# Kernel optimization log

Hardware: AMD Instinct MI355X
Metric: run time of the kernel (lower is better)

The kernel has to match this reference:

```python
import jax, jax.numpy as jnp
import numpy as np

N = 50000      # nodes
E = 1_600_000  # edges (avg degree 32)
IN, H, OUT, R = 128, 64, 32, 8
NEG_SLOPE = 0.2


def _rgat(x, src, dst, etype, W, q, k, b, n_nodes):
    """PyG RGATConv, defaults: heads=1, dim=1, additive-self-attention,
    across-relation softmax, concat=True, bias=True, dropout=0 (eval)."""
    # per-relation transform of all nodes: [R, N, O] (cheaper than per-edge bmm since 2*deg >> R)
    t = jnp.einsum('ni,rio->rno', x, W)
    xi = t[etype, dst]                      # [E, O] transformed target feats
    xj = t[etype, src]                      # [E, O] transformed source feats
    a = (xi @ q + xj @ k)[:, 0]             # [E] additive attention logits
    a = jnp.where(a >= 0, a, NEG_SLOPE * a)  # leaky_relu
    # segment softmax over incoming edges of each target node (across relations)
    m = jax.ops.segment_max(a, dst, num_segments=n_nodes)
    m = jnp.where(jnp.isfinite(m), m, 0.0)
    ex = jnp.exp(a - m[dst])
    s = jax.ops.segment_sum(ex, dst, num_segments=n_nodes)
    alpha = ex / (s[dst] + 1e-16)
    out = jax.ops.segment_sum(alpha[:, None] * xj, dst, num_segments=n_nodes)
    return out + b


def setup_inputs() -> dict:
    key = jax.random.key(0)
    ks = jax.random.split(key, 24)
    x = jax.random.normal(ks[0], (N, IN), jnp.float32)
    edge_index = jax.random.randint(ks[1], (2, E), 0, N, jnp.int32)
    edge_type = jax.random.randint(ks[2], (E,), 0, R, jnp.int32)

    def glorot(k, shape, fan_in):
        return jax.random.normal(k, shape, jnp.float32) * (1.0 / np.sqrt(fan_in))

    d = dict(x=x, edge_index=edge_index, edge_type=edge_type)
    # conv1: in->hidden, conv_mu / conv_logvar: hidden->hidden
    d['W1'] = glorot(ks[3], (R, IN, H), IN)
    d['q1'] = glorot(ks[4], (H, 1), H)
    d['k1'] = glorot(ks[5], (H, 1), H)
    d['b1'] = jnp.zeros((H,), jnp.float32)
    d['Wmu'] = glorot(ks[6], (R, H, H), H)
    d['qmu'] = glorot(ks[7], (H, 1), H)
    d['kmu'] = glorot(ks[8], (H, 1), H)
    d['bmu'] = jnp.zeros((H,), jnp.float32)
    d['Wlv'] = glorot(ks[9], (R, H, H), H)
    d['qlv'] = glorot(ks[10], (H, 1), H)
    d['klv'] = glorot(ks[11], (H, 1), H)
    d['blv'] = jnp.zeros((H,), jnp.float32)
    d['Wm'] = glorot(ks[12], (H, OUT), H)   # linear_mu (stored [in,out])
    d['bm'] = jnp.zeros((OUT,), jnp.float32)
    d['Wl'] = glorot(ks[13], (H, OUT), H)   # linear_logvar
    d['bl'] = jnp.zeros((OUT,), jnp.float32)
    return d


def reference(x, edge_index, edge_type, W1, q1, k1, b1,
              Wmu, qmu, kmu, bmu, Wlv, qlv, klv, blv, Wm, bm, Wl, bl):
    src, dst = edge_index[0], edge_index[1]
    hidden = jax.nn.relu(_rgat(x, src, dst, edge_type, W1, q1, k1, b1, N))
    mu = jax.nn.relu(_rgat(hidden, src, dst, edge_type, Wmu, qmu, kmu, bmu, N))
    mu = mu @ Wm + bm                       # dropout is identity in eval
    logvar = jax.nn.relu(_rgat(hidden, src, dst, edge_type, Wlv, qlv, klv, blv, N))
    logvar = logvar @ Wl + bl
    logstd = 0.5 * logvar
    return (mu, logstd)
```

## Files before the change

### kernel.cpp

```cpp
#include <hip/hip_runtime.h>
#include <cstdint>

#define HDIM 64
#define ODIM 32
#define NEG_SLOPE 0.2f
#define SCHUNK 2048
#define EPB 8192

typedef __attribute__((ext_vector_type(8))) short v8s;
typedef __attribute__((ext_vector_type(4))) float v4f;

__device__ __forceinline__ unsigned f2bf_rne(float f) {
  unsigned u = __float_as_uint(f);
  return (u + 0x7FFFu + ((u >> 16) & 1u)) >> 16;
}

__device__ __forceinline__ unsigned fenc(float f) {
  unsigned u = __float_as_uint(f);
  return (u & 0x80000000u) ? ~u : (u | 0x80000000u);
}
__device__ __forceinline__ float fdec(unsigned e) {
  unsigned u = (e & 0x80000000u) ? (e ^ 0x80000000u) : ~e;
  return __uint_as_float(u);
}

__global__ __launch_bounds__(256) void cvt_bf16_kernel(
    const float* __restrict__ in, unsigned short* __restrict__ out, int n) {
  int i = (blockIdx.x * 256 + threadIdx.x) * 4;
  if (i + 3 < n) {
    float4 v = *(const float4*)&in[i];
    ushort4 o;
    o.x = (unsigned short)f2bf_rne(v.x);
    o.y = (unsigned short)f2bf_rne(v.y);
    o.z = (unsigned short)f2bf_rne(v.z);
    o.w = (unsigned short)f2bf_rne(v.w);
    *(ushort4*)&out[i] = o;
  }
}

__global__ __launch_bounds__(256) void transpose_w_kernel(
    const float* __restrict__ W1, const float* __restrict__ Wmu,
    const float* __restrict__ Wlv, unsigned short* __restrict__ W1t,
    unsigned short* __restrict__ Wmut, unsigned short* __restrict__ Wlvt) {
  const int b = blockIdx.x;
  const int r = b & 7;
  const int which = b >> 3;
  const float* src;
  unsigned short* dst;
  int K;
  if (which == 0) {
    src = W1; dst = W1t; K = 128;
  } else if (which == 1) {
    src = Wmu; dst = Wmut; K = 64;
  } else {
    src = Wlv; dst = Wlvt; K = 64;
  }
  for (int idx = threadIdx.x; idx < K * 64; idx += 256) {
    const int kk = idx >> 6, o = idx & 63;
    dst[((size_t)r * 64 + o) * K + kk] =
        (unsigned short)f2bf_rne(src[((size_t)r * K + kk) * 64 + o]);
  }
}

__global__ __launch_bounds__(256) void count_deg_kernel(
    const int* __restrict__ dst, int* __restrict__ deg, int E) {
  int e = blockIdx.x * 256 + threadIdx.x;
  if (e < E) atomicAdd(&deg[dst[e]], 1);
}

__global__ __launch_bounds__(256) void scan_p1(const int* __restrict__ deg,
                                               int* __restrict__ bsum, int n) {
  int base = blockIdx.x * SCHUNK + threadIdx.x * 8;
  int s = 0;
#pragma unroll
  for (int j = 0; j < 8; j++) {
    int i = base + j;
    if (i < n) s += deg[i];
  }
#pragma unroll
  for (int d = 1; d < 64; d <<= 1) s += __shfl_xor(s, d, 64);
  __shared__ int ws[4];
  if ((threadIdx.x & 63) == 0) ws[threadIdx.x >> 6] = s;
  __syncthreads();
  if (threadIdx.x == 0) bsum[blockIdx.x] = ws[0] + ws[1] + ws[2] + ws[3];
}

__global__ void scan_p2(int* bsum, int nb) {
  int i = threadIdx.x;
  int v = (i < nb) ? bsum[i] : 0;
  int orig = v;
#pragma unroll
  for (int d = 1; d < 64; d <<= 1) {
    int up = __shfl_up(v, d, 64);
    if (i >= d) v += up;
  }
  if (i < nb) bsum[i] = v - orig;
}

__global__ __launch_bounds__(256) void scan_p3(const int* __restrict__ deg,
                                               const int* __restrict__ bsum,
                                               int* __restrict__ row_ptr,
                                               int n) {
  int base = blockIdx.x * SCHUNK + threadIdx.x * 8;
  int vals[8];
  int s = 0;
#pragma unroll
  for (int j = 0; j < 8; j++) {
    int i = base + j;
    vals[j] = (i < n) ? deg[i] : 0;
    s += vals[j];
  }
  int lane = threadIdx.x & 63, w = threadIdx.x >> 6;
  int v = s;
#pragma unroll
  for (int d = 1; d < 64; d <<= 1) {
    int up = __shfl_up(v, d, 64);
    if (lane >= d) v += up;
  }
  __shared__ int wsum[4];
  if (lane == 63) wsum[w] = v;
  __syncthreads();
  int woff = 0;
#pragma unroll
  for (int i = 0; i < 4; i++) woff += (i < w) ? wsum[i] : 0;
  int off = bsum[blockIdx.x] + woff + v - s;
#pragma unroll
  for (int j = 0; j < 8; j++) {
    int i = base + j;
    off += vals[j];
    if (i < n) row_ptr[i + 1] = off;
  }
  if (blockIdx.x == 0 && threadIdx.x == 0) row_ptr[0] = 0;
}

__global__ __launch_bounds__(256) void bucket_cursor_init(
    const int* __restrict__ row_ptr, int* __restrict__ cursor, int N, int nb) {
  int i = threadIdx.x;
  if (i < nb) cursor[i] = row_ptr[min(i * 256, N)];
}

__global__ __launch_bounds__(256) void bucket_pass1(
    const int* __restrict__ src, const int* __restrict__ dst,
    const int* __restrict__ etype, int* __restrict__ cursor,
    unsigned* __restrict__ tmp, int E) {
  __shared__ int hist[256];
  __shared__ int binstart[256];
  __shared__ int gbase[256];
  __shared__ int fill[256];
  __shared__ int wsum[4];
  __shared__ unsigned stage[EPB];
  __shared__ unsigned char binof[EPB];
  const int tid = threadIdx.x;
  const int e0 = blockIdx.x * EPB;
  const int cnt = min(EPB, E - e0);

  hist[tid] = 0;
  fill[tid] = 0;
  __syncthreads();
  for (int j = tid; j < cnt; j += 256) atomicAdd(&hist[dst[e0 + j] >> 8], 1);
  __syncthreads();

  const int hv = hist[tid];
  {
    const int lane = tid & 63, w = tid >> 6;
    int iv = hv;
#pragma unroll
    for (int d = 1; d < 64; d <<= 1) {
      int up = __shfl_up(iv, d, 64);
      if (lane >= d) iv += up;
    }
    if (lane == 63) wsum[w] = iv;
    __syncthreads();
    int woff = 0;
#pragma unroll
    for (int i = 0; i < 4; i++) woff += (i < w) ? wsum[i] : 0;
    binstart[tid] = woff + iv - hv;
    if (hv > 0) gbase[tid] = atomicAdd(&cursor[tid], hv);
  }
  __syncthreads();

  for (int j = tid; j < cnt; j += 256) {
    const int d = dst[e0 + j];
    const int b = d >> 8;
    const unsigned rec = ((unsigned)(d & 255) << 19) |
                         ((unsigned)etype[e0 + j] << 16) |
                         (unsigned)src[e0 + j];
    const int slot = binstart[b] + atomicAdd(&fill[b], 1);
    stage[slot] = rec;
    binof[slot] = (unsigned char)b;
  }
  __syncthreads();

  for (int s = tid; s < cnt; s += 256) {
    const int b = binof[s];
    tmp[gbase[b] + (s - binstart[b])] = stage[s];
  }
}

__global__ __launch_bounds__(256) void bucket_pass2(
    const int* __restrict__ row_ptr, const unsigned* __restrict__ tmp,
    int* __restrict__ edges, int N) {
  __shared__ int rp[257];
  __shared__ int fill[256];
  const int tid = threadIdx.x;
  const int rowbase = blockIdx.x * 256;
  const int rowcnt = min(256, N - rowbase);
  for (int i = tid; i <= rowcnt; i += 256) rp[i] = row_ptr[rowbase + i];
  fill[tid] = 0;
  __syncthreads();
  const int beg = rp[0];
  const int endv = rp[rowcnt];
  for (int i = beg + tid; i < endv; i += 256) {
    const unsigned rec = tmp[i];
    const int dlow = rec >> 19;
    const int pos = rp[dlow] + atomicAdd(&fill[dlow], 1);
    edges[pos] = (int)(rec & 0x7FFFFu);
  }
}

__global__ __launch_bounds__(256) void rowmax_kernel(
    const float* __restrict__ ak, unsigned* __restrict__ maxk_enc, int N) {
  const int row = blockIdx.x;
  const int nchunks = gridDim.y;
  const int per = (N + nchunks - 1) / nchunks;
  const int beg = blockIdx.y * per;
  const int end = min(N, beg + per);
  const float* r = ak + (size_t)row * N;
  float m = -1e30f;
  for (int i = beg + threadIdx.x; i < end; i += 256) m = fmaxf(m, r[i]);
#pragma unroll
  for (int d = 1; d < 64; d <<= 1) m = fmaxf(m, __shfl_xor(m, d, 64));
  __shared__ float ws[4];
  if ((threadIdx.x & 63) == 0) ws[threadIdx.x >> 6] = m;
  __syncthreads();
  if (threadIdx.x == 0) {
    float bm = fmaxf(fmaxf(ws[0], ws[1]), fmaxf(ws[2], ws[3]));
    atomicMax(&maxk_enc[row], fenc(bm));
  }
}

__global__ __launch_bounds__(256) void transform1_mfma(
    const unsigned short* __restrict__ xb,
    const unsigned short* __restrict__ W1t, const float* __restrict__ q,
    const float* __restrict__ k, unsigned short* __restrict__ tb,
    float* __restrict__ aq, float* __restrict__ ak, int N) {
  __shared__ unsigned short st[4][16][72];
  const int r = blockIdx.x;
  const int tid = threadIdx.x;
  const int w = tid >> 6;
  const int lane = tid & 63;
  const int quad = lane >> 4;
  const int mrow = lane & 15;
  const int n0w = blockIdx.y * 64 + w * 16;

  const int gA = min(n0w + mrow, N - 1);
  const unsigned short* arow = xb + (size_t)gA * 128 + quad * 8;
  const unsigned short* wrow = W1t + ((size_t)r * 64 + mrow) * 128 + quad * 8;

  v4f acc[4];
#pragma unroll
  for (int tt = 0; tt < 4; tt++) acc[tt] = (v4f){0.f, 0.f, 0.f, 0.f};

#pragma unroll
  for (int k0 = 0; k0 < 128; k0 += 32) {
    v8s a = *(const v8s*)(arow + k0);
#pragma unroll
    for (int tt = 0; tt < 4; tt++) {
      v8s b = *(const v8s*)(wrow + (size_t)tt * 16 * 128 + k0);
      acc[tt] = __builtin_amdgcn_mfma_f32_16x16x32_bf16(a, b, acc[tt], 0, 0, 0);
    }
  }

  float qv[4], kv[4];
#pragma unroll
  for (int tt = 0; tt < 4; tt++) {
    qv[tt] = q[tt * 16 + mrow];
    kv[tt] = k[tt * 16 + mrow];
  }

#pragma unroll
  for (int i = 0; i < 4; i++) {
    float vq = 0.f, vk = 0.f;
#pragma unroll
    for (int tt = 0; tt < 4; tt++) {
      vq = fmaf(acc[tt][i], qv[tt], vq);
      vk = fmaf(acc[tt][i], kv[tt], vk);
      st[w][quad * 4 + i][tt * 16 + mrow] =
          (unsigned short)f2bf_rne(acc[tt][i]);
    }
#pragma unroll
    for (int d = 1; d < 16; d <<= 1) {
      vq += __shfl_xor(vq, d, 64);
      vk += __shfl_xor(vk, d, 64);
    }
    const int gn = n0w + quad * 4 + i;
    if (mrow == 0 && gn < N) {
      aq[(size_t)r * N + gn] = vq;
      ak[(size_t)r * N + gn] = vk;
    }
  }
  __syncthreads();

  const int row = lane >> 2, cg = lane & 3;
  const int gns = n0w + row;
  if (gns < N) {
    const uint4 v0 = *(const uint4*)&st[w][row][cg * 16];
    const uint4 v1 = *(const uint4*)&st[w][row][cg * 16 + 8];
    uint4* dst = (uint4*)&tb[((size_t)r * N + gns) * 64 + cg * 16];
    dst[0] = v0;
    dst[1] = v1;
  }
}

__global__ __launch_bounds__(256) void transform2_mfma(
    const unsigned short* __restrict__ hb,
    const unsigned short* __restrict__ Wmut,
    const unsigned short* __restrict__ Wlvt, const float* __restrict__ qa,
    const float* __restrict__ ka, const float* __restrict__ qb,
    const float* __restrict__ kb, unsigned* __restrict__ t2p,
    float* __restrict__ aq2, float* __restrict__ ak2, int N) {
  __shared__ unsigned st2[4][16][68];
  const int r = blockIdx.x;
  const int tid = threadIdx.x;
  const int w = tid >> 6;
  const int lane = tid & 63;
  const int quad = lane >> 4;
  const int mrow = lane & 15;
  const int n0w = blockIdx.y * 64 + w * 16;

  const int gA = min(n0w + mrow, N - 1);
  const unsigned short* arow = hb + (size_t)gA * 64 + quad * 8;
  const size_t woff = ((size_t)r * 64 + mrow) * 64 + quad * 8;

  v4f am[4], al[4];
#pragma unroll
  for (int tt = 0; tt < 4; tt++) {
    am[tt] = (v4f){0.f, 0.f, 0.f, 0.f};
    al[tt] = (v4f){0.f, 0.f, 0.f, 0.f};
  }

#pragma unroll
  for (int k0 = 0; k0 < 64; k0 += 32) {
    v8s a = *(const v8s*)(arow + k0);
#pragma unroll
    for (int tt = 0; tt < 4; tt++) {
      v8s bm = *(const v8s*)(Wmut + woff + (size_t)tt * 16 * 64 + k0);
      v8s bl = *(const v8s*)(Wlvt + woff + (size_t)tt * 16 * 64 + k0);
      am[tt] = __builtin_amdgcn_mfma_f32_16x16x32_bf16(a, bm, am[tt], 0, 0, 0);
      al[tt] = __builtin_amdgcn_mfma_f32_16x16x32_bf16(a, bl, al[tt], 0, 0, 0);
    }
  }

  float qmv[4], kmv[4], qlv2[4], klv2[4];
#pragma unroll
  for (int tt = 0; tt < 4; tt++) {
    qmv[tt] = qa[tt * 16 + mrow];
    kmv[tt] = ka[tt * 16 + mrow];
    qlv2[tt] = qb[tt * 16 + mrow];
    klv2[tt] = kb[tt * 16 + mrow];
  }

#pragma unroll
  for (int i = 0; i < 4; i++) {
    float vqm = 0.f, vkm = 0.f, vql = 0.f, vkl = 0.f;
#pragma unroll
    for (int tt = 0; tt < 4; tt++) {
      vqm = fmaf(am[tt][i], qmv[tt], vqm);
      vkm = fmaf(am[tt][i], kmv[tt], vkm);
      vql = fmaf(al[tt][i], qlv2[tt], vql);
      vkl = fmaf(al[tt][i], klv2[tt], vkl);
      st2[w][quad * 4 + i][tt * 16 + mrow] =
          f2bf_rne(am[tt][i]) | (f2bf_rne(al[tt][i]) << 16);
    }
#pragma unroll
    for (int d = 1; d < 16; d <<= 1) {
      vqm += __shfl_xor(vqm, d, 64);
      vkm += __shfl_xor(vkm, d, 64);
      vql += __shfl_xor(vql, d, 64);
      vkl += __shfl_xor(vkl, d, 64);
    }
    const int gn = n0w + quad * 4 + i;
    if (mrow == 0 && gn < N) {
      aq2[(size_t)r * N + gn] = vqm;
      ak2[(size_t)r * N + gn] = vkm;
      aq2[(size_t)(8 + r) * N + gn] = vql;
      ak2[(size_t)(8 + r) * N + gn] = vkl;
    }
  }
  __syncthreads();

  const int row = lane >> 2, cg = lane & 3;
  const int gns = n0w + row;
  if (gns < N) {
    unsigned* dst = &t2p[((size_t)r * N + gns) * 64 + cg * 16];
#pragma unroll
    for (int s = 0; s < 4; s++)
      *(uint4*)(dst + s * 4) = *(const uint4*)&st2[w][row][cg * 16 + s * 4];
  }
}

__global__ __launch_bounds__(256) void aggregate_kernel(
    const int* __restrict__ row_ptr, const int* __restrict__ edges,
    const unsigned short* __restrict__ tb, const float* __restrict__ aq,
    const float* __restrict__ ak, const unsigned* __restrict__ maxk_enc,
    const float* __restrict__ bias, unsigned short* __restrict__ hb, int N) {
  const int tid = threadIdx.x;
  const int w = tid >> 6, o = tid & 63;
  int wid = blockIdx.x * 4 + w;
  const bool valid = wid < N;
  if (!valid) wid = N - 1;
  const int beg = row_ptr[wid];
  const int end = valid ? row_ptr[wid + 1] : beg;
  const int deg = end - beg;

  const float aqw = aq[(size_t)(o & 7) * N + wid];

  float v = aqw + fdec(maxk_enc[o & 7]);
  v = (v >= 0.f) ? v : NEG_SLOPE * v;
#pragma unroll
  for (int d = 1; d < 8; d <<= 1) v = fmaxf(v, __shfl_xor(v, d, 64));
  const float m = __shfl(v, 0, 64);

  const int g = o >> 3;
  const int cl = o & 7;
  float s = 0.f;
  float acc[8];
#pragma unroll
  for (int c = 0; c < 8; c++) acc[c] = 0.f;

  for (int base = 0; base < deg; base += 64) {
    const int j = base + o;
    const int gcount = min(64, deg - base);
    const int packed = edges[beg + min(j, deg - 1)];
    const int src = packed & 0xFFFF;
    const int rr = packed >> 16;
    const int idx = rr * N + src;
    float x = __shfl(aqw, rr, 64) + ak[idx];
    x = (x >= 0.f) ? x : NEG_SLOPE * x;
    const float p = (j < deg) ? __expf(x - m) : 0.f;
    s += p;
    const int g8 = (gcount + 7) & ~7;
#pragma unroll 4
    for (int u = 0; u < g8; u += 8) {
      const int e = u + g;
      const float pe = __shfl(p, e, 64);
      const int ie = __shfl(idx, e, 64);
      const uint4 tv = *(const uint4*)(tb + (size_t)ie * 64 + cl * 8);
      const unsigned uu0 = tv.x, uu1 = tv.y, uu2 = tv.z, uu3 = tv.w;
      acc[0] = fmaf(pe, __uint_as_float(uu0 << 16), acc[0]);
      acc[1] = fmaf(pe, __uint_as_float(uu0 & 0xFFFF0000u), acc[1]);
      acc[2] = fmaf(pe, __uint_as_float(uu1 << 16), acc[2]);
      acc[3] = fmaf(pe, __uint_as_float(uu1 & 0xFFFF0000u), acc[3]);
      acc[4] = fmaf(pe, __uint_as_float(uu2 << 16), acc[4]);
      acc[5] = fmaf(pe, __uint_as_float(uu2 & 0xFFFF0000u), acc[5]);
      acc[6] = fmaf(pe, __uint_as_float(uu3 << 16), acc[6]);
      acc[7] = fmaf(pe, __uint_as_float(uu3 & 0xFFFF0000u), acc[7]);
    }
  }
#pragma unroll
  for (int d = 1; d < 64; d <<= 1) s += __shfl_xor(s, d, 64);
#pragma unroll
  for (int d = 8; d < 64; d <<= 1) {
#pragma unroll
    for (int c = 0; c < 8; c++) acc[c] += __shfl_xor(acc[c], d, 64);
  }

  if (valid && g == 0) {
    const float inv = 1.f / (s + 1e-16f);
    unsigned rv[8];
#pragma unroll
    for (int c = 0; c < 8; c++) {
      const float res = acc[c] * inv + bias[cl * 8 + c];
      rv[c] = f2bf_rne(fmaxf(res, 0.f));
    }
    uint4 pkd;
    pkd.x = rv[0] | (rv[1] << 16);
    pkd.y = rv[2] | (rv[3] << 16);
    pkd.z = rv[4] | (rv[5] << 16);
    pkd.w = rv[6] | (rv[7] << 16);
    *(uint4*)(hb + (size_t)wid * 64 + cl * 8) = pkd;
  }
}

__global__ __launch_bounds__(256) void aggregate2_kernel(
    const int* __restrict__ row_ptr, const int* __restrict__ edges,
    const unsigned* __restrict__ t2p, const float* __restrict__ aq2,
    const float* __restrict__ ak2, const unsigned* __restrict__ maxk2_enc,
    const float* __restrict__ bmu, const float* __restrict__ blv,
    const float* __restrict__ Wm, const float* __restrict__ bm,
    const float* __restrict__ Wlin, const float* __restrict__ bl,
    float* __restrict__ out_mu, float* __restrict__ out_ls, int N) {
  __shared__ float WmL[2048];
  __shared__ float WlL[2048];
  __shared__ float bL[64];
  __shared__ float hL[4][130];
  const int tid = threadIdx.x;
  for (int i = tid; i < 2048; i += 256) {
    WmL[i] = Wm[i];
    WlL[i] = Wlin[i];
  }
  if (tid < 32) {
    bL[tid] = bm[tid];
    bL[32 + tid] = bl[tid];
  }
  __syncthreads();

  const int w = tid >> 6, o = tid & 63;
  int wid = blockIdx.x * 4 + w;
  const bool valid = wid < N;
  if (!valid) wid = N - 1;
  const int beg = row_ptr[wid];
  const int end = valid ? row_ptr[wid + 1] : beg;
  const int deg = end - beg;

  const float aqw = aq2[(size_t)(o & 15) * N + wid];

  float v = aqw + fdec(maxk2_enc[o & 15]);
  v = (v >= 0.f) ? v : NEG_SLOPE * v;
#pragma unroll
  for (int d = 1; d < 8; d <<= 1) v = fmaxf(v, __shfl_xor(v, d, 64));
  const float m0 = __shfl(v, 0, 64);
  const float m1 = __shfl(v, 8, 64);

  const int g = o >> 4;
  const int cl = o & 15;
  float s0 = 0.f, s1 = 0.f;
  float acc0[4], acc1[4];
#pragma unroll
  for (int c = 0; c < 4; c++) {
    acc0[c] = 0.f;
    acc1[c] = 0.f;
  }

  for (int base = 0; base < deg; base += 64) {
    const int j = base + o;
    const int gcount = min(64, deg - base);
    const int packed = edges[beg + min(j, deg - 1)];
    const int src = packed & 0xFFFF;
    const int rr = packed >> 16;
    const int idx = rr * N + src;
    float x0 = __shfl(aqw, rr, 64) + ak2[idx];
    float x1 = __shfl(aqw, 8 + rr, 64) + ak2[idx + 8 * N];
    x0 = (x0 >= 0.f) ? x0 : NEG_SLOPE * x0;
    x1 = (x1 >= 0.f) ? x1 : NEG_SLOPE * x1;
    const float p0 = (j < deg) ? __expf(x0 - m0) : 0.f;
    const float p1 = (j < deg) ? __expf(x1 - m1) : 0.f;
    s0 += p0;
    s1 += p1;
    const int g4 = (gcount + 3) & ~3;
#pragma unroll 4
    for (int u = 0; u < g4; u += 4) {
      const int e = u + g;
      const float pe0 = __shfl(p0, e, 64);
      const float pe1 = __shfl(p1, e, 64);
      const int ie = __shfl(idx, e, 64);
      const uint4 pk = *(const uint4*)(t2p + (size_t)ie * 64 + cl * 4);
      const unsigned uu0 = pk.x, uu1 = pk.y, uu2 = pk.z, uu3 = pk.w;
      acc0[0] = fmaf(pe0, __uint_as_float(uu0 << 16), acc0[0]);
      acc1[0] = fmaf(pe1, __uint_as_float(uu0 & 0xFFFF0000u), acc1[0]);
      acc0[1] = fmaf(pe0, __uint_as_float(uu1 << 16), acc0[1]);
      acc1[1] = fmaf(pe1, __uint_as_float(uu1 & 0xFFFF0000u), acc1[1]);
      acc0[2] = fmaf(pe0, __uint_as_float(uu2 << 16), acc0[2]);
      acc1[2] = fmaf(pe1, __uint_as_float(uu2 & 0xFFFF0000u), acc1[2]);
      acc0[3] = fmaf(pe0, __uint_as_float(uu3 << 16), acc0[3]);
      acc1[3] = fmaf(pe1, __uint_as_float(uu3 & 0xFFFF0000u), acc1[3]);
    }
  }
#pragma unroll
  for (int d = 1; d < 64; d <<= 1) {
    s0 += __shfl_xor(s0, d, 64);
    s1 += __shfl_xor(s1, d, 64);
  }
#pragma unroll
  for (int d = 16; d < 64; d <<= 1) {
#pragma unroll
    for (int c = 0; c < 4; c++) {
      acc0[c] += __shfl_xor(acc0[c], d, 64);
      acc1[c] += __shfl_xor(acc1[c], d, 64);
    }
  }

  if (g == 0) {
    const float inv0 = 1.f / (s0 + 1e-16f);
    const float inv1 = 1.f / (s1 + 1e-16f);
#pragma unroll
    for (int c = 0; c < 4; c++) {
      hL[w][cl * 4 + c] = fmaxf(acc0[c] * inv0 + bmu[cl * 4 + c], 0.f);
      hL[w][64 + cl * 4 + c] = fmaxf(acc1[c] * inv1 + blv[cl * 4 + c], 0.f);
    }
  }
  __syncthreads();

  const float* hrow = &hL[w][(o >= 32) ? 64 : 0];
  const float* WL = (o >= 32) ? WlL : WmL;
  const int j = o & 31;
  float acc = 0.f;
#pragma unroll 8
  for (int c = 0; c < 64; c++) acc = fmaf(hrow[c], WL[c * 32 + j], acc);
  if (valid) {
    if (o < 32)
      out_mu[(size_t)wid * 32 + j] = acc + bL[j];
    else
      out_ls[(size_t)wid * 32 + j] = (acc + bL[32 + j]) * 0.5f;
  }
}

extern "C" void kernel_launch(void* const* d_in, const int* in_sizes, int n_in,
                              void* d_out, int out_size, void* d_ws,
                              size_t ws_size, hipStream_t stream) {
  const float* x = (const float*)d_in[0];
  const int* edge_index = (const int*)d_in[1];
  const int* edge_type = (const int*)d_in[2];
  const float* W1 = (const float*)d_in[3];
  const float* q1 = (const float*)d_in[4];
  const float* k1 = (const float*)d_in[5];
  const float* b1 = (const float*)d_in[6];
  const float* Wmu = (const float*)d_in[7];
  const float* qmu = (const float*)d_in[8];
  const float* kmu = (const float*)d_in[9];
  const float* bmu = (const float*)d_in[10];
  const float* Wlv = (const float*)d_in[11];
  const float* qlv = (const float*)d_in[12];
  const float* klv = (const float*)d_in[13];
  const float* blv = (const float*)d_in[14];
  const float* Wm = (const float*)d_in[15];
  const float* bm = (const float*)d_in[16];
  const float* Wl = (const float*)d_in[17];
  const float* bl = (const float*)d_in[18];

  const int N = in_sizes[0] / 128;
  const int E = in_sizes[2];
  const int R = in_sizes[3] / (128 * 64);

  float* out_mu = (float*)d_out;
  float* out_ls = (float*)d_out + (size_t)N * ODIM;

  char* wsp = (char*)d_ws;
  size_t off = 0;
  auto carve = [&](size_t bytes) {
    void* p = wsp + off;
    off += (bytes + 255) & ~(size_t)255;
    return p;
  };

  void* tbuf = carve((size_t)R * N * 64 * sizeof(unsigned));
  unsigned short* t1b = (unsigned short*)tbuf;
  unsigned* t2p = (unsigned*)tbuf;
  unsigned short* xb = (unsigned short*)carve((size_t)N * 128 * 2);
  unsigned short* hb = (unsigned short*)carve((size_t)N * 64 * 2);
  unsigned short* W1t = (unsigned short*)carve((size_t)R * 64 * 128 * 2);
  unsigned short* Wmut = (unsigned short*)carve((size_t)R * 64 * 64 * 2);
  unsigned short* Wlvt = (unsigned short*)carve((size_t)R * 64 * 64 * 2);
  float* aq2 = (float*)carve((size_t)2 * R * N * sizeof(float));
  float* ak2 = (float*)carve((size_t)2 * R * N * sizeof(float));
  unsigned* maxk_enc = (unsigned*)carve(2 * R * sizeof(unsigned));
  int* deg = (int*)carve((size_t)N * sizeof(int));
  int* row_ptr = (int*)carve((size_t)(N + 1) * sizeof(int));
  int* bsum = (int*)carve(256 * sizeof(int));
  int* cursor = (int*)carve(256 * sizeof(int));
  unsigned* tmp = (unsigned*)carve((size_t)E * sizeof(unsigned));
  int* edges = (int*)carve((size_t)E * sizeof(int));

  const int* e_src = edge_index;
  const int* e_dst = edge_index + E;

  cvt_bf16_kernel<<<(N * 128 / 4 + 255) / 256, 256, 0, stream>>>(x, xb,
                                                                 N * 128);
  transpose_w_kernel<<<3 * R, 256, 0, stream>>>(W1, Wmu, Wlv, W1t, Wmut, Wlvt);

  hipMemsetAsync(deg, 0, (size_t)N * sizeof(int), stream);
  hipMemsetAsync(maxk_enc, 0, 2 * R * sizeof(unsigned), stream);
  count_deg_kernel<<<(E + 255) / 256, 256, 0, stream>>>(e_dst, deg, E);
  const int nchunk = (N + SCHUNK - 1) / SCHUNK;
  scan_p1<<<nchunk, 256, 0, stream>>>(deg, bsum, N);
  scan_p2<<<1, 64, 0, stream>>>(bsum, nchunk);
  scan_p3<<<nchunk, 256, 0, stream>>>(deg, bsum, row_ptr, N);

  const int nbuck = (N + 255) >> 8;
  bucket_cursor_init<<<1, 256, 0, stream>>>(row_ptr, cursor, N, nbuck);
  bucket_pass1<<<(E + EPB - 1) / EPB, 256, 0, stream>>>(e_src, e_dst,
                                                        edge_type, cursor,
                                                        tmp, E);
  bucket_pass2<<<nbuck, 256, 0, stream>>>(row_ptr, tmp, edges, N);

  const int nb64 = (N + 63) / 64;
  const int agg_blocks = (N + 3) / 4;

  transform1_mfma<<<dim3(R, nb64), 256, 0, stream>>>(xb, W1t, q1, k1, t1b,
                                                     aq2, ak2, N);
  rowmax_kernel<<<dim3(R, 32), 256, 0, stream>>>(ak2, maxk_enc, N);
  aggregate_kernel<<<agg_blocks, 256, 0, stream>>>(
      row_ptr, edges, t1b, aq2, ak2, maxk_enc, b1, hb, N);

  hipMemsetAsync(maxk_enc, 0, 2 * R * sizeof(unsigned), stream);

  transform2_mfma<<<dim3(R, nb64), 256, 0, stream>>>(
      hb, Wmut, Wlvt, qmu, kmu, qlv, klv, t2p, aq2, ak2, N);
  rowmax_kernel<<<dim3(2 * R, 32), 256, 0, stream>>>(ak2, maxk_enc, N);
  aggregate2_kernel<<<agg_blocks, 256, 0, stream>>>(
      row_ptr, edges, t2p, aq2, ak2, maxk_enc, bmu, blv, Wm, bm, Wl, bl,
      out_mu, out_ls, N);
}
```

Measured before the change: 554.6 us.

## Aggregate raw hidden features per relation before transforming layer-2 outputs

The CSR is now sorted by (dst, relation), so layer 2 aggregates the 64-wide bf16 hidden rows per relation instead of gathering per-relation transformed features. The weight transform moves after aggregation and runs as a single 512-K MFMA GEMM over the concatenated per-relation sums. Attention logits come directly from hidden via precomputed W·q and W·k vectors. This drops the large R×N transformed-feature buffer and its gather traffic. In exchange it adds an N×8 degree scan, a larger 8-relation y buffer and an extra kernel.

```diff
diff --git a/kernel.cpp b/kernel.cpp
--- a/kernel.cpp
+++ b/kernel.cpp
@@ -41,31 +41,48 @@
 __global__ __launch_bounds__(256) void transpose_w_kernel(
     const float* __restrict__ W1, const float* __restrict__ Wmu,
     const float* __restrict__ Wlv, unsigned short* __restrict__ W1t,
-    unsigned short* __restrict__ Wmut, unsigned short* __restrict__ Wlvt) {
+    unsigned short* __restrict__ Wct) {
   const int b = blockIdx.x;
-  const int r = b & 7;
-  const int which = b >> 3;
-  const float* src;
-  unsigned short* dst;
-  int K;
-  if (which == 0) {
-    src = W1; dst = W1t; K = 128;
-  } else if (which == 1) {
-    src = Wmu; dst = Wmut; K = 64;
+  if (b < 8) {
+    const int r = b;
+    for (int idx = threadIdx.x; idx < 128 * 64; idx += 256) {
+      const int kk = idx >> 6, o = idx & 63;
+      W1t[((size_t)r * 64 + o) * 128 + kk] =
+          (unsigned short)f2bf_rne(W1[((size_t)r * 128 + kk) * 64 + o]);
+    }
   } else {
-    src = Wlv; dst = Wlvt; K = 64;
-  }
-  for (int idx = threadIdx.x; idx < K * 64; idx += 256) {
-    const int kk = idx >> 6, o = idx & 63;
-    dst[((size_t)r * 64 + o) * K + kk] =
-        (unsigned short)f2bf_rne(src[((size_t)r * K + kk) * 64 + o]);
+    const int s = (b - 8) >> 3, r = (b - 8) & 7;
+    const float* src = s ? Wlv : Wmu;
+    for (int idx = threadIdx.x; idx < 64 * 64; idx += 256) {
+      const int kk = idx >> 6, o = idx & 63;
+      Wct[((size_t)s * 64 + o) * 512 + r * 64 + kk] =
+          (unsigned short)f2bf_rne(src[((size_t)r * 64 + kk) * 64 + o]);
+    }
+  }
+}
+
+__global__ __launch_bounds__(256) void prep_T_kernel(
+    const float* __restrict__ Wmu, const float* __restrict__ qmu,
+    const float* __restrict__ kmu, const float* __restrict__ Wlv,
+    const float* __restrict__ qlv, const float* __restrict__ klv,
+    float* __restrict__ T) {
+  for (int idx = threadIdx.x; idx < 2048; idx += 256) {
+    const int j = idx >> 6, c = idx & 63;
+    const int isk = j >> 4, sr = j & 15, s = sr >> 3, r = sr & 7;
+    const float* W = s ? Wlv : Wmu;
+    const float* vec = s ? (isk ? klv : qlv) : (isk ? kmu : qmu);
+    float acc = 0.f;
+    for (int o = 0; o < 64; o++)
+      acc += W[((size_t)r * 64 + c) * 64 + o] * vec[o];
+    T[idx] = acc;
   }
 }
 
 __global__ __launch_bounds__(256) void count_deg_kernel(
-    const int* __restrict__ dst, int* __restrict__ deg, int E) {
+    const int* __restrict__ dst, const int* __restrict__ etype,
+    int* __restrict__ deg, int E) {
   int e = blockIdx.x * 256 + threadIdx.x;
-  if (e < E) atomicAdd(&deg[dst[e]], 1);
+  if (e < E) atomicAdd(&deg[dst[e] * 8 + etype[e]], 1);
 }
 
 __global__ __launch_bounds__(256) void scan_p1(const int* __restrict__ deg,
@@ -85,16 +102,23 @@
   if (threadIdx.x == 0) bsum[blockIdx.x] = ws[0] + ws[1] + ws[2] + ws[3];
 }
 
-__global__ void scan_p2(int* bsum, int nb) {
-  int i = threadIdx.x;
+__global__ __launch_bounds__(256) void scan_p2(int* bsum, int nb) {
+  __shared__ int wsum[4];
+  const int i = threadIdx.x;
   int v = (i < nb) ? bsum[i] : 0;
-  int orig = v;
+  const int orig = v;
+  const int lane = i & 63, w = i >> 6;
 #pragma unroll
   for (int d = 1; d < 64; d <<= 1) {
     int up = __shfl_up(v, d, 64);
-    if (i >= d) v += up;
-  }
-  if (i < nb) bsum[i] = v - orig;
+    if (lane >= d) v += up;
+  }
+  if (lane == 63) wsum[w] = v;
+  __syncthreads();
+  int woff = 0;
+#pragma unroll
+  for (int k = 0; k < 4; k++) woff += (k < w) ? wsum[k] : 0;
+  if (i < nb) bsum[i] = woff + v - orig;
 }
 
 __global__ __launch_bounds__(256) void scan_p3(const int* __restrict__ deg,
@@ -134,9 +158,9 @@
 }
 
 __global__ __launch_bounds__(256) void bucket_cursor_init(
-    const int* __restrict__ row_ptr, int* __restrict__ cursor, int N, int nb) {
+    const int* __restrict__ rp2, int* __restrict__ cursor, int N, int nb) {
   int i = threadIdx.x;
-  if (i < nb) cursor[i] = row_ptr[min(i * 256, N)];
+  if (i < nb) cursor[i] = rp2[(size_t)min(i * 256, N) * 8];
 }
 
 __global__ __launch_bounds__(256) void bucket_pass1(
@@ -198,22 +222,22 @@
 }
 
 __global__ __launch_bounds__(256) void bucket_pass2(
-    const int* __restrict__ row_ptr, const unsigned* __restrict__ tmp,
+    const int* __restrict__ rp2, const unsigned* __restrict__ tmp,
     int* __restrict__ edges, int N) {
-  __shared__ int rp[257];
-  __shared__ int fill[256];
+  __shared__ int rp[2049];
+  __shared__ int fill[2048];
   const int tid = threadIdx.x;
   const int rowbase = blockIdx.x * 256;
   const int rowcnt = min(256, N - rowbase);
-  for (int i = tid; i <= rowcnt; i += 256) rp[i] = row_ptr[rowbase + i];
-  fill[tid] = 0;
+  for (int i = tid; i <= rowcnt * 8; i += 256) rp[i] = rp2[(size_t)rowbase * 8 + i];
+  for (int i = tid; i < 2048; i += 256) fill[i] = 0;
   __syncthreads();
   const int beg = rp[0];
-  const int endv = rp[rowcnt];
+  const int endv = rp[rowcnt * 8];
   for (int i = beg + tid; i < endv; i += 256) {
     const unsigned rec = tmp[i];
-    const int dlow = rec >> 19;
-    const int pos = rp[dlow] + atomicAdd(&fill[dlow], 1);
+    const int bin = rec >> 16;
+    const int pos = rp[bin] + atomicAdd(&fill[bin], 1);
     edges[pos] = (int)(rec & 0x7FFFFu);
   }
 }
@@ -312,95 +336,8 @@
   }
 }
 
-__global__ __launch_bounds__(256) void transform2_mfma(
-    const unsigned short* __restrict__ hb,
-    const unsigned short* __restrict__ Wmut,
-    const unsigned short* __restrict__ Wlvt, const float* __restrict__ qa,
-    const float* __restrict__ ka, const float* __restrict__ qb,
-    const float* __restrict__ kb, unsigned* __restrict__ t2p,
-    float* __restrict__ aq2, float* __restrict__ ak2, int N) {
-  __shared__ unsigned st2[4][16][68];
-  const int r = blockIdx.x;
-  const int tid = threadIdx.x;
-  const int w = tid >> 6;
-  const int lane = tid & 63;
-  const int quad = lane >> 4;
-  const int mrow = lane & 15;
-  const int n0w = blockIdx.y * 64 + w * 16;
-
-  const int gA = min(n0w + mrow, N - 1);
-  const unsigned short* arow = hb + (size_t)gA * 64 + quad * 8;
-  const size_t woff = ((size_t)r * 64 + mrow) * 64 + quad * 8;
-
-  v4f am[4], al[4];
-#pragma unroll
-  for (int tt = 0; tt < 4; tt++) {
-    am[tt] = (v4f){0.f, 0.f, 0.f, 0.f};
-    al[tt] = (v4f){0.f, 0.f, 0.f, 0.f};
-  }
-
-#pragma unroll
-  for (int k0 = 0; k0 < 64; k0 += 32) {
-    v8s a = *(const v8s*)(arow + k0);
-#pragma unroll
-    for (int tt = 0; tt < 4; tt++) {
-      v8s bm = *(const v8s*)(Wmut + woff + (size_t)tt * 16 * 64 + k0);
-      v8s bl = *(const v8s*)(Wlvt + woff + (size_t)tt * 16 * 64 + k0);
-      am[tt] = __builtin_amdgcn_mfma_f32_16x16x32_bf16(a, bm, am[tt], 0, 0, 0);
-      al[tt] = __builtin_amdgcn_mfma_f32_16x16x32_bf16(a, bl, al[tt], 0, 0, 0);
-    }
-  }
-
-  float qmv[4], kmv[4], qlv2[4], klv2[4];
-#pragma unroll
-  for (int tt = 0; tt < 4; tt++) {
-    qmv[tt] = qa[tt * 16 + mrow];
-    kmv[tt] = ka[tt * 16 + mrow];
-    qlv2[tt] = qb[tt * 16 + mrow];
-    klv2[tt] = kb[tt * 16 + mrow];
-  }
-
-#pragma unroll
-  for (int i = 0; i < 4; i++) {
-    float vqm = 0.f, vkm = 0.f, vql = 0.f, vkl = 0.f;
-#pragma unroll
-    for (int tt = 0; tt < 4; tt++) {
-      vqm = fmaf(am[tt][i], qmv[tt], vqm);
-      vkm = fmaf(am[tt][i], kmv[tt], vkm);
-      vql = fmaf(al[tt][i], qlv2[tt], vql);
-      vkl = fmaf(al[tt][i], klv2[tt], vkl);
-      st2[w][quad * 4 + i][tt * 16 + mrow] =
-          f2bf_rne(am[tt][i]) | (f2bf_rne(al[tt][i]) << 16);
-    }
-#pragma unroll
-    for (int d = 1; d < 16; d <<= 1) {
-      vqm += __shfl_xor(vqm, d, 64);
-      vkm += __shfl_xor(vkm, d, 64);
-      vql += __shfl_xor(vql, d, 64);
-      vkl += __shfl_xor(vkl, d, 64);
-    }
-    const int gn = n0w + quad * 4 + i;
-    if (mrow == 0 && gn < N) {
-      aq2[(size_t)r * N + gn] = vqm;
-      ak2[(size_t)r * N + gn] = vkm;
-      aq2[(size_t)(8 + r) * N + gn] = vql;
-      ak2[(size_t)(8 + r) * N + gn] = vkl;
-    }
-  }
-  __syncthreads();
-
-  const int row = lane >> 2, cg = lane & 3;
-  const int gns = n0w + row;
-  if (gns < N) {
-    unsigned* dst = &t2p[((size_t)r * N + gns) * 64 + cg * 16];
-#pragma unroll
-    for (int s = 0; s < 4; s++)
-      *(uint4*)(dst + s * 4) = *(const uint4*)&st2[w][row][cg * 16 + s * 4];
-  }
-}
-
 __global__ __launch_bounds__(256) void aggregate_kernel(
-    const int* __restrict__ row_ptr, const int* __restrict__ edges,
+    const int* __restrict__ rp2, const int* __restrict__ edges,
     const unsigned short* __restrict__ tb, const float* __restrict__ aq,
     const float* __restrict__ ak, const unsigned* __restrict__ maxk_enc,
     const float* __restrict__ bias, unsigned short* __restrict__ hb, int N) {
@@ -409,8 +346,8 @@
   int wid = blockIdx.x * 4 + w;
   const bool valid = wid < N;
   if (!valid) wid = N - 1;
-  const int beg = row_ptr[wid];
-  const int end = valid ? row_ptr[wid + 1] : beg;
+  const int beg = rp2[(size_t)wid * 8];
+  const int end = valid ? rp2[(size_t)wid * 8 + 8] : beg;
   const int deg = end - beg;
 
   const float aqw = aq[(size_t)(o & 7) * N + wid];
@@ -440,7 +377,6 @@
     const float p = (j < deg) ? __expf(x - m) : 0.f;
     s += p;
     const int g8 = (gcount + 7) & ~7;
-#pragma unroll 4
     for (int u = 0; u < g8; u += 8) {
       const int e = u + g;
       const float pe = __shfl(p, e, 64);
@@ -482,39 +418,58 @@
   }
 }
 
-__global__ __launch_bounds__(256) void aggregate2_kernel(
-    const int* __restrict__ row_ptr, const int* __restrict__ edges,
-    const unsigned* __restrict__ t2p, const float* __restrict__ aq2,
+__global__ __launch_bounds__(256) void logit2_kernel(
+    const unsigned short* __restrict__ hb, const float* __restrict__ T,
+    float* __restrict__ aq2, float* __restrict__ ak2, int N) {
+  __shared__ float Ts[2048];
+  for (int i = threadIdx.x; i < 2048; i += 256) Ts[i] = T[i];
+  __syncthreads();
+  const int n = blockIdx.x * 256 + threadIdx.x;
+  if (n >= N) return;
+  float h[64];
+  const unsigned short* hr = hb + (size_t)n * 64;
+#pragma unroll
+  for (int d = 0; d < 8; d++) {
+    const uint4 u = *(const uint4*)(hr + d * 8);
+    h[d * 8 + 0] = __uint_as_float(u.x << 16);
+    h[d * 8 + 1] = __uint_as_float(u.x & 0xFFFF0000u);
+    h[d * 8 + 2] = __uint_as_float(u.y << 16);
+    h[d * 8 + 3] = __uint_as_float(u.y & 0xFFFF0000u);
+    h[d * 8 + 4] = __uint_as_float(u.z << 16);
+    h[d * 8 + 5] = __uint_as_float(u.z & 0xFFFF0000u);
+    h[d * 8 + 6] = __uint_as_float(u.w << 16);
+    h[d * 8 + 7] = __uint_as_float(u.w & 0xFFFF0000u);
+  }
+#pragma unroll
+  for (int j = 0; j < 16; j++) {
+    float dq = 0.f, dk = 0.f;
+#pragma unroll
+    for (int c = 0; c < 64; c++) {
+      dq = fmaf(h[c], Ts[j * 64 + c], dq);
+      dk = fmaf(h[c], Ts[(16 + j) * 64 + c], dk);
+    }
+    aq2[(size_t)j * N + n] = dq;
+    ak2[(size_t)j * N + n] = dk;
+  }
+}
+
+__global__ __launch_bounds__(256) void aggregate2h_kernel(
+    const int* __restrict__ rp2, const int* __restrict__ edges,
+    const unsigned short* __restrict__ hb, const float* __restrict__ aq2,
     const float* __restrict__ ak2, const unsigned* __restrict__ maxk2_enc,
-    const float* __restrict__ bmu, const float* __restrict__ blv,
-    const float* __restrict__ Wm, const float* __restrict__ bm,
-    const float* __restrict__ Wlin, const float* __restrict__ bl,
-    float* __restrict__ out_mu, float* __restrict__ out_ls, int N) {
-  __shared__ float WmL[2048];
-  __shared__ float WlL[2048];
-  __shared__ float bL[64];
-  __shared__ float hL[4][130];
+    unsigned* __restrict__ y, float* __restrict__ sbuf, int N) {
+  __shared__ float sred[2][2];
   const int tid = threadIdx.x;
-  for (int i = tid; i < 2048; i += 256) {
-    WmL[i] = Wm[i];
-    WlL[i] = Wlin[i];
-  }
-  if (tid < 32) {
-    bL[tid] = bm[tid];
-    bL[32 + tid] = bl[tid];
-  }
-  __syncthreads();
-
   const int w = tid >> 6, o = tid & 63;
-  int wid = blockIdx.x * 4 + w;
+  const int nl = w >> 1;
+  const int rbase = (w & 1) * 4;
+  int wid = blockIdx.x * 2 + nl;
   const bool valid = wid < N;
   if (!valid) wid = N - 1;
-  const int beg = row_ptr[wid];
-  const int end = valid ? row_ptr[wid + 1] : beg;
-  const int deg = end - beg;
+  if (tid < 4) ((float*)sred)[tid] = 0.f;
+  __syncthreads();
 
   const float aqw = aq2[(size_t)(o & 15) * N + wid];
-
   float v = aqw + fdec(maxk2_enc[o & 15]);
   v = (v >= 0.f) ? v : NEG_SLOPE * v;
 #pragma unroll
@@ -522,86 +477,147 @@
   const float m0 = __shfl(v, 0, 64);
   const float m1 = __shfl(v, 8, 64);
 
-  const int g = o >> 4;
-  const int cl = o & 15;
+  const int g = o >> 5;
+  const int k = o & 31;
   float s0 = 0.f, s1 = 0.f;
-  float acc0[4], acc1[4];
-#pragma unroll
-  for (int c = 0; c < 4; c++) {
-    acc0[c] = 0.f;
-    acc1[c] = 0.f;
-  }
-
-  for (int base = 0; base < deg; base += 64) {
-    const int j = base + o;
-    const int gcount = min(64, deg - base);
-    const int packed = edges[beg + min(j, deg - 1)];
-    const int src = packed & 0xFFFF;
-    const int rr = packed >> 16;
-    const int idx = rr * N + src;
-    float x0 = __shfl(aqw, rr, 64) + ak2[idx];
-    float x1 = __shfl(aqw, 8 + rr, 64) + ak2[idx + 8 * N];
-    x0 = (x0 >= 0.f) ? x0 : NEG_SLOPE * x0;
-    x1 = (x1 >= 0.f) ? x1 : NEG_SLOPE * x1;
-    const float p0 = (j < deg) ? __expf(x0 - m0) : 0.f;
-    const float p1 = (j < deg) ? __expf(x1 - m1) : 0.f;
-    s0 += p0;
-    s1 += p1;
-    const int g4 = (gcount + 3) & ~3;
-#pragma unroll 4
-    for (int u = 0; u < g4; u += 4) {
-      const int e = u + g;
-      const float pe0 = __shfl(p0, e, 64);
-      const float pe1 = __shfl(p1, e, 64);
-      const int ie = __shfl(idx, e, 64);
-      const uint4 pk = *(const uint4*)(t2p + (size_t)ie * 64 + cl * 4);
-      const unsigned uu0 = pk.x, uu1 = pk.y, uu2 = pk.z, uu3 = pk.w;
-      acc0[0] = fmaf(pe0, __uint_as_float(uu0 << 16), acc0[0]);
-      acc1[0] = fmaf(pe1, __uint_as_float(uu0 & 0xFFFF0000u), acc1[0]);
-      acc0[1] = fmaf(pe0, __uint_as_float(uu1 << 16), acc0[1]);
-      acc1[1] = fmaf(pe1, __uint_as_float(uu1 & 0xFFFF0000u), acc1[1]);
-      acc0[2] = fmaf(pe0, __uint_as_float(uu2 << 16), acc0[2]);
-      acc1[2] = fmaf(pe1, __uint_as_float(uu2 & 0xFFFF0000u), acc1[2]);
-      acc0[3] = fmaf(pe0, __uint_as_float(uu3 << 16), acc0[3]);
-      acc1[3] = fmaf(pe1, __uint_as_float(uu3 & 0xFFFF0000u), acc1[3]);
-    }
-  }
+  float aE0[4], aO0[4], aE1[4], aO1[4];
+#pragma unroll
+  for (int r = 0; r < 4; r++) {
+    aE0[r] = 0.f;
+    aO0[r] = 0.f;
+    aE1[r] = 0.f;
+    aO1[r] = 0.f;
+  }
+
+  const size_t segbase = (size_t)wid * 8 + rbase;
+#pragma unroll
+  for (int r = 0; r < 4; r++) {
+    const int sb = rp2[segbase + r];
+    const int se = rp2[segbase + r + 1];
+    if (valid && sb < se) {
+      const float aqr0 = __shfl(aqw, rbase + r, 64);
+      const float aqr1 = __shfl(aqw, 8 + rbase + r, 64);
+      for (int base = sb; base < se; base += 64) {
+        const int j = base + o;
+        const int cnt = min(64, se - base);
+        const int src = edges[min(j, se - 1)] & 0xFFFF;
+        const float akv0 = ak2[(size_t)(rbase + r) * N + src];
+        const float akv1 = ak2[(size_t)(8 + rbase + r) * N + src];
+        float x0 = aqr0 + akv0;
+        float x1 = aqr1 + akv1;
+        x0 = (x0 >= 0.f) ? x0 : NEG_SLOPE * x0;
+        x1 = (x1 >= 0.f) ? x1 : NEG_SLOPE * x1;
+        const float p0 = (j < se) ? __expf(x0 - m0) : 0.f;
+        const float p1 = (j < se) ? __expf(x1 - m1) : 0.f;
+        s0 += p0;
+        s1 += p1;
+        for (int u = 0; 2 * u < cnt; u++) {
+          const int e = 2 * u + g;
+          const float pe0 = __shfl(p0, e, 64);
+          const float pe1 = __shfl(p1, e, 64);
+          const int ie = __shfl(src, e, 64);
+          const unsigned hw =
+              *(const unsigned*)(hb + (size_t)ie * 64 + k * 2);
+          const float h0 = __uint_as_float(hw << 16);
+          const float h1 = __uint_as_float(hw & 0xFFFF0000u);
+          aE0[r] = fmaf(pe0, h0, aE0[r]);
+          aO0[r] = fmaf(pe0, h1, aO0[r]);
+          aE1[r] = fmaf(pe1, h0, aE1[r]);
+          aO1[r] = fmaf(pe1, h1, aO1[r]);
+        }
+      }
+    }
+  }
+
 #pragma unroll
   for (int d = 1; d < 64; d <<= 1) {
     s0 += __shfl_xor(s0, d, 64);
     s1 += __shfl_xor(s1, d, 64);
   }
 #pragma unroll
-  for (int d = 16; d < 64; d <<= 1) {
-#pragma unroll
-    for (int c = 0; c < 4; c++) {
-      acc0[c] += __shfl_xor(acc0[c], d, 64);
-      acc1[c] += __shfl_xor(acc1[c], d, 64);
-    }
-  }
-
-  if (g == 0) {
-    const float inv0 = 1.f / (s0 + 1e-16f);
-    const float inv1 = 1.f / (s1 + 1e-16f);
-#pragma unroll
-    for (int c = 0; c < 4; c++) {
-      hL[w][cl * 4 + c] = fmaxf(acc0[c] * inv0 + bmu[cl * 4 + c], 0.f);
-      hL[w][64 + cl * 4 + c] = fmaxf(acc1[c] * inv1 + blv[cl * 4 + c], 0.f);
-    }
-  }
-  __syncthreads();
-
-  const float* hrow = &hL[w][(o >= 32) ? 64 : 0];
-  const float* WL = (o >= 32) ? WlL : WmL;
-  const int j = o & 31;
-  float acc = 0.f;
-#pragma unroll 8
-  for (int c = 0; c < 64; c++) acc = fmaf(hrow[c], WL[c * 32 + j], acc);
-  if (valid) {
-    if (o < 32)
-      out_mu[(size_t)wid * 32 + j] = acc + bL[j];
-    else
-      out_ls[(size_t)wid * 32 + j] = (acc + bL[32 + j]) * 0.5f;
+  for (int r = 0; r < 4; r++) {
+    aE0[r] += __shfl_xor(aE0[r], 32, 64);
+    aO0[r] += __shfl_xor(aO0[r], 32, 64);
+    aE1[r] += __shfl_xor(aE1[r], 32, 64);
+    aO1[r] += __shfl_xor(aO1[r], 32, 64);
+  }
+  if (valid && o == 0) {
+    atomicAdd(&sred[nl][0], s0);
+    atomicAdd(&sred[nl][1], s1);
+  }
+  if (valid && g == 0) {
+#pragma unroll
+    for (int r = 0; r < 4; r++) {
+      const unsigned u0 = f2bf_rne(aE0[r]) | (f2bf_rne(aO0[r]) << 16);
+      const unsigned u1 = f2bf_rne(aE1[r]) | (f2bf_rne(aO1[r]) << 16);
+      y[(size_t)wid * 256 + (rbase + r) * 32 + k] = u0;
+      y[((size_t)N + wid) * 256 + (rbase + r) * 32 + k] = u1;
+    }
+  }
+  __syncthreads();
+  if (valid && o == 0 && rbase == 0) {
+    sbuf[(size_t)wid * 2 + 0] = sred[nl][0];
+    sbuf[(size_t)wid * 2 + 1] = sred[nl][1];
+  }
+}
+
+__global__ __launch_bounds__(256) void out2_kernel(
+    const unsigned short* __restrict__ yb,
+    const unsigned short* __restrict__ Wct, const float* __restrict__ sbuf,
+    const float* __restrict__ bmu, const float* __restrict__ blv,
+    const float* __restrict__ Wm, const float* __restrict__ bm,
+    const float* __restrict__ Wl, const float* __restrict__ bl,
+    float* __restrict__ out_mu, float* __restrict__ out_ls, int N) {
+  __shared__ float hstf[64][65];
+  __shared__ float WL[2048];
+  __shared__ float b2L[32];
+  const int s = blockIdx.y;
+  const int tid = threadIdx.x;
+  for (int i = tid; i < 2048; i += 256) WL[i] = s ? Wl[i] : Wm[i];
+  if (tid < 32) b2L[tid] = s ? bl[tid] : bm[tid];
+
+  const int w = tid >> 6, lane = tid & 63;
+  const int quad = lane >> 4, mrow = lane & 15;
+  const int n0w = blockIdx.x * 64 + w * 16;
+  const int gA = min(n0w + mrow, N - 1);
+  const unsigned short* arow = yb + ((size_t)s * N + gA) * 512 + quad * 8;
+  const unsigned short* wrow = Wct + ((size_t)s * 64 + mrow) * 512 + quad * 8;
+
+  v4f acc[4];
+#pragma unroll
+  for (int tt = 0; tt < 4; tt++) acc[tt] = (v4f){0.f, 0.f, 0.f, 0.f};
+#pragma unroll
+  for (int k0 = 0; k0 < 512; k0 += 32) {
+    v8s a = *(const v8s*)(arow + k0);
+#pragma unroll
+    for (int tt = 0; tt < 4; tt++) {
+      v8s b = *(const v8s*)(wrow + (size_t)tt * 16 * 512 + k0);
+      acc[tt] = __builtin_amdgcn_mfma_f32_16x16x32_bf16(a, b, acc[tt], 0, 0, 0);
+    }
+  }
+
+  const float* bc = s ? blv : bmu;
+#pragma unroll
+  for (int i = 0; i < 4; i++) {
+    const int node = min(n0w + quad * 4 + i, N - 1);
+    const float inv = 1.f / (sbuf[(size_t)node * 2 + s] + 1e-16f);
+#pragma unroll
+    for (int tt = 0; tt < 4; tt++) {
+      hstf[w * 16 + quad * 4 + i][tt * 16 + mrow] =
+          fmaxf(acc[tt][i] * inv + bc[tt * 16 + mrow], 0.f);
+    }
+  }
+  __syncthreads();
+
+  const float mul = s ? 0.5f : 1.f;
+  float* outp = s ? out_ls : out_mu;
+  for (int idx = tid; idx < 2048; idx += 256) {
+    const int nl2 = idx >> 5, oo = idx & 31;
+    const int node = blockIdx.x * 64 + nl2;
+    float a2 = 0.f;
+#pragma unroll
+    for (int c = 0; c < 64; c++) a2 = fmaf(hstf[nl2][c], WL[c * 32 + oo], a2);
+    if (node < N) outp[(size_t)node * 32 + oo] = (a2 + b2L[oo]) * mul;
   }
 }
 
@@ -645,17 +661,19 @@
 
   void* tbuf = carve((size_t)R * N * 64 * sizeof(unsigned));
   unsigned short* t1b = (unsigned short*)tbuf;
-  unsigned* t2p = (unsigned*)tbuf;
+  unsigned short* yb = (unsigned short*)tbuf;
+  unsigned* yw = (unsigned*)tbuf;
   unsigned short* xb = (unsigned short*)carve((size_t)N * 128 * 2);
   unsigned short* hb = (unsigned short*)carve((size_t)N * 64 * 2);
   unsigned short* W1t = (unsigned short*)carve((size_t)R * 64 * 128 * 2);
-  unsigned short* Wmut = (unsigned short*)carve((size_t)R * 64 * 64 * 2);
-  unsigned short* Wlvt = (unsigned short*)carve((size_t)R * 64 * 64 * 2);
+  unsigned short* Wct = (unsigned short*)carve((size_t)2 * 64 * 512 * 2);
+  float* Tdir = (float*)carve((size_t)32 * 64 * sizeof(float));
   float* aq2 = (float*)carve((size_t)2 * R * N * sizeof(float));
   float* ak2 = (float*)carve((size_t)2 * R * N * sizeof(float));
   unsigned* maxk_enc = (unsigned*)carve(2 * R * sizeof(unsigned));
-  int* deg = (int*)carve((size_t)N * sizeof(int));
-  int* row_ptr = (int*)carve((size_t)(N + 1) * sizeof(int));
+  float* sbuf = (float*)carve((size_t)N * 2 * sizeof(float));
+  int* deg = (int*)carve((size_t)N * 8 * sizeof(int));
+  int* rp2 = (int*)carve(((size_t)N * 8 + 1) * sizeof(int));
   int* bsum = (int*)carve(256 * sizeof(int));
   int* cursor = (int*)carve(256 * sizeof(int));
   unsigned* tmp = (unsigned*)carve((size_t)E * sizeof(unsigned));
@@ -666,38 +684,41 @@
 
   cvt_bf16_kernel<<<(N * 128 / 4 + 255) / 256, 256, 0, stream>>>(x, xb,
                                                                  N * 128);
-  transpose_w_kernel<<<3 * R, 256, 0, stream>>>(W1, Wmu, Wlv, W1t, Wmut, Wlvt);
-
-  hipMemsetAsync(deg, 0, (size_t)N * sizeof(int), stream);
+  transpose_w_kernel<<<24, 256, 0, stream>>>(W1, Wmu, Wlv, W1t, Wct);
+  prep_T_kernel<<<1, 256, 0, stream>>>(Wmu, qmu, kmu, Wlv, qlv, klv, Tdir);
+
+  hipMemsetAsync(deg, 0, (size_t)N * 8 * sizeof(int), stream);
   hipMemsetAsync(maxk_enc, 0, 2 * R * sizeof(unsigned), stream);
-  count_deg_kernel<<<(E + 255) / 256, 256, 0, stream>>>(e_dst, deg, E);
-  const int nchunk = (N + SCHUNK - 1) / SCHUNK;
-  scan_p1<<<nchunk, 256, 0, stream>>>(deg, bsum, N);
-  scan_p2<<<1, 64, 0, stream>>>(bsum, nchunk);
-  scan_p3<<<nchunk, 256, 0, stream>>>(deg, bsum, row_ptr, N);
+  count_deg_kernel<<<(E + 255) / 256, 256, 0, stream>>>(e_dst, edge_type, deg,
+                                                        E);
+  const int n2 = N * 8;
+  const int nchunk = (n2 + SCHUNK - 1) / SCHUNK;
+  scan_p1<<<nchunk, 256, 0, stream>>>(deg, bsum, n2);
+  scan_p2<<<1, 256, 0, stream>>>(bsum, nchunk);
+  scan_p3<<<nchunk, 256, 0, stream>>>(deg, bsum, rp2, n2);
 
   const int nbuck = (N + 255) >> 8;
-  bucket_cursor_init<<<1, 256, 0, stream>>>(row_ptr, cursor, N, nbuck);
+  bucket_cursor_init<<<1, 256, 0, stream>>>(rp2, cursor, N, nbuck);
   bucket_pass1<<<(E + EPB - 1) / EPB, 256, 0, stream>>>(e_src, e_dst,
                                                         edge_type, cursor,
                                                         tmp, E);
-  bucket_pass2<<<nbuck, 256, 0, stream>>>(row_ptr, tmp, edges, N);
+  bucket_pass2<<<nbuck, 256, 0, stream>>>(rp2, tmp, edges, N);
 
   const int nb64 = (N + 63) / 64;
-  const int agg_blocks = (N + 3) / 4;
 
   transform1_mfma<<<dim3(R, nb64), 256, 0, stream>>>(xb, W1t, q1, k1, t1b,
                                                      aq2, ak2, N);
   rowmax_kernel<<<dim3(R, 32), 256, 0, stream>>>(ak2, maxk_enc, N);
-  aggregate_kernel<<<agg_blocks, 256, 0, stream>>>(
-      row_ptr, edges, t1b, aq2, ak2, maxk_enc, b1, hb, N);
-
+  aggregate_kernel<<<(N + 3) / 4, 256, 0, stream>>>(rp2, edges, t1b, aq2, ak2,
+                                                    maxk_enc, b1, hb, N);
+
+  logit2_kernel<<<(N + 255) / 256, 256, 0, stream>>>(hb, Tdir, aq2, ak2, N);
   hipMemsetAsync(maxk_enc, 0, 2 * R * sizeof(unsigned), stream);
-
-  transform2_mfma<<<dim3(R, nb64), 256, 0, stream>>>(
-      hb, Wmut, Wlvt, qmu, kmu, qlv, klv, t2p, aq2, ak2, N);
   rowmax_kernel<<<dim3(2 * R, 32), 256, 0, stream>>>(ak2, maxk_enc, N);
-  aggregate2_kernel<<<agg_blocks, 256, 0, stream>>>(
-      row_ptr, edges, t2p, aq2, ak2, maxk_enc, bmu, blv, Wm, bm, Wl, bl,
-      out_mu, out_ls, N);
-}
+  aggregate2h_kernel<<<(N + 1) / 2, 256, 0, stream>>>(rp2, edges, hb, aq2,
+                                                      ak2, maxk_enc, yw, sbuf,
+                                                      N);
+  out2_kernel<<<dim3(nb64, 2), 256, 0, stream>>>(yb, Wct, sbuf, bmu, blv, Wm,
+                                                 bm, Wl, bl, out_mu, out_ls,
+                                                 N);
+}
```

Measured after the change: 609.4 us. +9.9%, slower.
